# Optimization experiments

Measured on AMD Instinct MI355X. Metric: run time of the kernel, lower is better.

Reference implementation:

```python
import jax, jax.numpy as jnp
import numpy as np

NUM_LAYERS = 3


def setup_inputs() -> dict:
    key = jax.random.key(0)
    k1, k2, k3 = jax.random.split(key, 3)
    B, LT, LC, F = 16, 256, 768, 256
    batch_target = jax.random.normal(k1, (B, LT, F), dtype=jnp.float32)
    batch_claim = jax.random.normal(k2, (B, LC, F), dtype=jnp.float32)
    # adjacency is accepted but mathematically unused (original masked_fill is non-in-place and discarded)
    batch_adj = jax.random.randint(jax.random.fold_in(key, 7), (B, LT + LC, LT + LC), 0, 2, dtype=jnp.int32)
    # per-layer trans_linear weights, nn.Linear(F, F, bias=False): y = x @ W.T, W is [out, in]
    W_trans = jax.random.normal(k3, (NUM_LAYERS, F, F), dtype=jnp.float32) * (1.0 / np.sqrt(F))
    return {"batch_target": batch_target, "batch_claim": batch_claim, "batch_adj": batch_adj, "W_trans": W_trans}


def _gcn_layer(node_rep, W):
    # dot attention: score[b,i,j] = <h_i, h_j>  (symmetric all-pairs dot product)
    # NOTE: original's masked_fill(batch_adj == 0, -1e9) is NOT in-place and its
    # result is discarded, so no masking is applied -- reproduced faithfully here.
    corr = jnp.einsum('bif,bjf->bij', node_rep, node_rep)
    attn = jax.nn.softmax(corr, axis=2)              # softmax over j (dim=2)
    trans = jnp.einsum('blf,gf->blg', node_rep, W)   # trans_linear (bias=False)
    node_out = jax.nn.relu(node_rep + jnp.einsum('bij,bjf->bif', attn, trans))
    return node_out, attn


def reference(batch_target, batch_claim, batch_adj, W_trans):
    target_len = batch_target.shape[1]
    node_rep = jnp.concatenate([batch_target, batch_claim], axis=1)  # [B, L, F]
    all_node_rep, all_corr_score = (), ()
    for i in range(NUM_LAYERS):
        node_rep, corr_score = _gcn_layer(node_rep, W_trans[i])
        all_node_rep = all_node_rep + (node_rep,)
        all_corr_score = all_corr_score + (corr_score,)
        # gcn_dropout: identity in eval mode
    target_rep = node_rep[:, :target_len, :]
    claim_rep = node_rep[:, target_len:, :]
    return (target_rep, claim_rep, all_node_rep, all_corr_score)
```

## Files before the change

### kernel.cpp

```cpp
#include <hip/hip_runtime.h>

typedef _Float16 h16;
typedef _Float16 h16x8 __attribute__((ext_vector_type(8)));
typedef _Float16 h16x4 __attribute__((ext_vector_type(4)));
typedef float    f32x4 __attribute__((ext_vector_type(4)));

#define NBATCH 16
#define LROWS  1024
#define FDIM   256

#define OFF_TGT 0ull
#define OFF_CLM 1048576ull
#define OFF_NR  4194304ull
#define OFF_AT  16777216ull

__device__ __forceinline__ void split2(float x, h16& h, h16& l) {
    h = (h16)x;
    l = (h16)(x - (float)h);
}

typedef const __attribute__((address_space(1))) void gvoid;
typedef __attribute__((address_space(3))) void lvoid;
__device__ __forceinline__ void gl_lds16(const void* g, void* l) {
    __builtin_amdgcn_global_load_lds((gvoid*)g, (lvoid*)l, 16, 0, 0);
}

__device__ const unsigned char TRI_I[36] = {
    0,0,0,0,0,0,0,0, 1,1,1,1,1,1,1, 2,2,2,2,2,2, 3,3,3,3,3, 4,4,4,4, 5,5,5, 6,6, 7};
__device__ const unsigned char TRI_J[36] = {
    0,1,2,3,4,5,6,7, 1,2,3,4,5,6,7, 2,3,4,5,6,7, 3,4,5,6,7, 4,5,6,7, 5,6,7, 6,7, 7};

__global__ __launch_bounds__(256) void convert_all(const float* __restrict__ tgt,
                                                   const float* __restrict__ clm,
                                                   const float* __restrict__ W,
                                                   h16* __restrict__ xh, h16* __restrict__ xl,
                                                   h16* __restrict__ wh) {
    int bid = blockIdx.x;
    if (bid < 4096) {
        size_t e = ((size_t)bid * 256 + threadIdx.x) * 4;
        int b  = (int)(e >> 18);
        int rf = (int)(e & 262143);
        int r  = rf >> 8, f = rf & 255;
        const float* src = (r < 256)
            ? tgt + ((size_t)b << 16) + ((size_t)r << 8) + f
            : clm + (size_t)b * 196608 + ((size_t)(r - 256) << 8) + f;
        f32x4 v = *(const f32x4*)src;
        h16x4 hv, lv;
#pragma unroll
        for (int j = 0; j < 4; ++j) { h16 hh, ll; split2(v[j], hh, ll); hv[j] = hh; lv[j] = ll; }
        *(h16x4*)(xh + e) = hv;
        *(h16x4*)(xl + e) = lv;
    } else {
        size_t e = ((size_t)(bid - 4096) * 256 + threadIdx.x) * 4;
        f32x4 v = *(const f32x4*)(W + e);
        h16x4 hv;
#pragma unroll
        for (int j = 0; j < 4; ++j) hv[j] = (h16)v[j];
        *(h16x4*)(wh + e) = hv;
    }
}

__global__ __launch_bounds__(256, 3) void gemm_ct(
    const h16* __restrict__ Xh, const h16* __restrict__ Xl,
    const h16* __restrict__ Wh,
    h16* __restrict__ Ptil, float2* __restrict__ part,
    h16* __restrict__ Th) {
    const int b = blockIdx.x & 15;
    const int u = blockIdx.x >> 4;
    const bool isCorr = u < 36;
    int it, jt;
    if (isCorr) { it = TRI_I[u]; jt = TRI_J[u]; }
    else        { int v = u - 36; it = v >> 1; jt = v & 1; }
    const int i0 = it * 128;
    const int j0 = jt * 128;
    const int t  = threadIdx.x;
    const int lane = t & 63, wid = t >> 6;
    const int wr = wid >> 1, wc = wid & 1;

    __shared__ alignas(16) char lds[32768];

    const size_t arow = ((size_t)b * LROWS + i0) * 256;
    const h16* bHp; const h16* bLp; size_t brow;
    if (isCorr) { bHp = Xh; bLp = Xl; brow = ((size_t)b * LROWS + j0) * 256; }
    else        { bHp = Wh; bLp = Xl; brow = (size_t)j0 * 256; }

    f32x4 acc[4][4];
#pragma unroll
    for (int i = 0; i < 4; ++i)
#pragma unroll
        for (int j = 0; j < 4; ++j) acc[i][j] = (f32x4){0.f, 0.f, 0.f, 0.f};

    const int grow = t >> 2;
    const int gq   = t & 3;

    for (int kt = 0; kt < 8; ++kt) {
        __syncthreads();
#pragma unroll
        for (int p = 0; p < 2; ++p) {
            int r = p * 64 + grow;
            size_t so = (size_t)r * 256 + kt * 32 + ((gq ^ ((r >> 1) & 3)) << 3);
            char* d = lds + p * 4096 + wid * 1024;
            gl_lds16(Xh + arow + so, d);
            gl_lds16(Xl + arow + so, d + 8192);
            gl_lds16(bHp + brow + so, d + 16384);
            if (isCorr) gl_lds16(bLp + brow + so, d + 24576);
        }
        __syncthreads();

        const int kq = lane >> 4;
        const int rA = wr * 64 + (lane & 15);
        const int rB = wc * 64 + (lane & 15);
        h16x8 ah[4], al[4], bh[4], bl[4];
#pragma unroll
        for (int mi = 0; mi < 4; ++mi) {
            int r   = rA + mi * 16;
            int off = r * 64 + ((kq ^ ((r >> 1) & 3)) << 4);
            ah[mi] = *(const h16x8*)(lds + off);
            al[mi] = *(const h16x8*)(lds + 8192 + off);
        }
#pragma unroll
        for (int nj = 0; nj < 4; ++nj) {
            int r   = rB + nj * 16;
            int off = r * 64 + ((kq ^ ((r >> 1) & 3)) << 4);
            bh[nj] = *(const h16x8*)(lds + 16384 + off);
            if (isCorr) bl[nj] = *(const h16x8*)(lds + 24576 + off);
        }
        __builtin_amdgcn_s_setprio(1);
#pragma unroll
        for (int mi = 0; mi < 4; ++mi)
#pragma unroll
            for (int nj = 0; nj < 4; ++nj) {
                acc[mi][nj] = __builtin_amdgcn_mfma_f32_16x16x32_f16(ah[mi], bh[nj], acc[mi][nj], 0, 0, 0);
                acc[mi][nj] = __builtin_amdgcn_mfma_f32_16x16x32_f16(al[mi], bh[nj], acc[mi][nj], 0, 0, 0);
                if (isCorr)
                    acc[mi][nj] = __builtin_amdgcn_mfma_f32_16x16x32_f16(ah[mi], bl[nj], acc[mi][nj], 0, 0, 0);
            }
        __builtin_amdgcn_s_setprio(0);
    }

    const int mBase = i0 + wr * 64;
    const int nBase = j0 + wc * 64;
    if (isCorr) {
        h16* Pb = Ptil + (size_t)b * LROWS * 1024;
        {
            const int chunk = jt * 2 + wc;
#pragma unroll
            for (int mi = 0; mi < 4; ++mi)
#pragma unroll
                for (int rg = 0; rg < 4; ++rg) {
                    float v0 = acc[mi][0][rg], v1 = acc[mi][1][rg];
                    float v2 = acc[mi][2][rg], v3 = acc[mi][3][rg];
                    float mx = fmaxf(fmaxf(v0, v1), fmaxf(v2, v3));
#pragma unroll
                    for (int off = 8; off >= 1; off >>= 1) mx = fmaxf(mx, __shfl_xor(mx, off, 64));
                    float e0 = __expf(v0 - mx), e1 = __expf(v1 - mx);
                    float e2 = __expf(v2 - mx), e3 = __expf(v3 - mx);
                    float s = e0 + e1 + e2 + e3;
#pragma unroll
                    for (int off = 8; off >= 1; off >>= 1) s += __shfl_xor(s, off, 64);
                    int row = mBase + mi * 16 + ((lane >> 4) * 4) + rg;
                    if ((lane & 15) == 0)
                        part[((size_t)b * 1024 + row) * 16 + chunk] = make_float2(mx, s);
                    size_t rb = (size_t)row * 1024 + nBase + (lane & 15);
                    Pb[rb]      = (h16)e0;
                    Pb[rb + 16] = (h16)e1;
                    Pb[rb + 32] = (h16)e2;
                    Pb[rb + 48] = (h16)e3;
                }
        }
        if (it != jt) {
            const int chunk = it * 2 + wr;
#pragma unroll
            for (int nj = 0; nj < 4; ++nj) {
                float mx = -3.0e38f;
#pragma unroll
                for (int mi = 0; mi < 4; ++mi)
#pragma unroll
                    for (int rg = 0; rg < 4; ++rg) mx = fmaxf(mx, acc[mi][nj][rg]);
                mx = fmaxf(mx, __shfl_xor(mx, 16, 64));
                mx = fmaxf(mx, __shfl_xor(mx, 32, 64));
                float s = 0.f;
                h16x4 pt[4];
#pragma unroll
                for (int mi = 0; mi < 4; ++mi)
#pragma unroll
                    for (int rg = 0; rg < 4; ++rg) {
                        float e = __expf(acc[mi][nj][rg] - mx);
                        s += e;
                        pt[mi][rg] = (h16)e;
                    }
                s += __shfl_xor(s, 16, 64);
                s += __shfl_xor(s, 32, 64);
                int n = nBase + nj * 16 + (lane & 15);
                if (lane < 16)
                    part[((size_t)b * 1024 + n) * 16 + chunk] = make_float2(mx, s);
                size_t nb = (size_t)n * 1024 + mBase + ((lane >> 4) * 4);
#pragma unroll
                for (int mi = 0; mi < 4; ++mi)
                    *(h16x4*)(Pb + nb + mi * 16) = pt[mi];
            }
        }
    } else {
#pragma unroll
        for (int mi = 0; mi < 4; ++mi)
#pragma unroll
            for (int nj = 0; nj < 4; ++nj) {
                int n  = nBase + nj * 16 + (lane & 15);
                int m0 = mBase + mi * 16 + ((lane >> 4) * 4);
                h16x4 hv;
#pragma unroll
                for (int rg = 0; rg < 4; ++rg) hv[rg] = (h16)acc[mi][nj][rg];
                size_t off = ((size_t)b * 256 + n) * 1024 + m0;
                *(h16x4*)(Th + off) = hv;
            }
    }
}

__global__ __launch_bounds__(256, 4) void gemm_pv(
    const h16* __restrict__ Ptil, const float2* __restrict__ part,
    float* __restrict__ At,
    const h16* __restrict__ Th,
    h16* __restrict__ Xh, h16* __restrict__ Xl,
    float* __restrict__ NodeOut, float* __restrict__ OutBase, int last) {
    const int id   = blockIdx.x;
    const int xcd  = id & 7, rest = id >> 3;
    const int b    = (xcd << 1) | (rest & 1);
    const int mt   = rest >> 1;
    const int i0   = mt * 32;
    const int t    = threadIdx.x;
    const int lane = t & 63, wid = t >> 6;
    const int wc   = wid;

    __shared__ alignas(16) char lds[38912];
    float* sc = (float*)(lds + 36864);

    if (t < 32) {
        const float2* pp = part + ((size_t)b * 1024 + i0 + t) * 16;
        float2 v[16];
        float M = -3.0e38f;
#pragma unroll
        for (int c = 0; c < 16; ++c) { v[c] = pp[c]; M = fmaxf(M, v[c].x); }
        float S = 0.f;
#pragma unroll
        for (int c = 0; c < 16; ++c) S += v[c].y * __expf(v[c].x - M);
        float inv = 1.0f / S;
#pragma unroll
        for (int c = 0; c < 16; ++c) sc[t * 16 + c] = __expf(v[c].x - M) * inv;
    }
    __syncthreads();

    const h16* Prow = Ptil + ((size_t)b * LROWS + i0) * 1024;
    float* Arow = At + ((size_t)b * LROWS + i0) * 1024;
    const size_t tbase = (size_t)b * 256 * 1024;

    const int ar = t >> 3;
    const int ac = t & 7;

    f32x4 acc[2][4];
#pragma unroll
    for (int i = 0; i < 2; ++i)
#pragma unroll
        for (int j = 0; j < 4; ++j) acc[i][j] = (f32x4){0.f, 0.f, 0.f, 0.f};

    for (int kt = 0; kt < 16; ++kt) {
        h16x8 pt = *(const h16x8*)(Prow + (size_t)ar * 1024 + kt * 64 + ac * 8);
        float s  = sc[ar * 16 + kt];
        __syncthreads();

#pragma unroll
        for (int itr = 0; itr < 8; ++itr) {
            int g = itr * 32 + ar;
            size_t so = tbase + (size_t)g * 1024 + kt * 64 + ((ac ^ (g & 7)) << 3);
            char* d = lds + 4096 + itr * 4096 + wid * 1024;
            gl_lds16(Th + so, d);
        }

        f32x4 plo, phi;
#pragma unroll
        for (int e = 0; e < 4; ++e) plo[e] = (float)pt[e] * s;
#pragma unroll
        for (int e = 0; e < 4; ++e) phi[e] = (float)pt[4 + e] * s;
        *(f32x4*)(Arow + (size_t)ar * 1024 + kt * 64 + ac * 8)     = plo;
        *(f32x4*)(Arow + (size_t)ar * 1024 + kt * 64 + ac * 8 + 4) = phi;
        h16x8 a16;
#pragma unroll
        for (int e = 0; e < 4; ++e) { a16[e] = (h16)plo[e]; a16[4 + e] = (h16)phi[e]; }
        *(h16x8*)(lds + ar * 128 + ((ac ^ (ar & 7)) << 4)) = a16;
        __syncthreads();

        const int kq = lane >> 4;
        __builtin_amdgcn_s_setprio(1);
#pragma unroll
        for (int s2 = 0; s2 < 2; ++s2) {
            h16x8 ah[2], bh[4];
#pragma unroll
            for (int mi = 0; mi < 2; ++mi) {
                int r = mi * 16 + (lane & 15);
                ah[mi] = *(const h16x8*)(lds + r * 128 + (((s2 * 4 + kq) ^ (r & 7)) << 4));
            }
#pragma unroll
            for (int nf = 0; nf < 4; ++nf) {
                int g = wc * 64 + nf * 16 + (lane & 15);
                bh[nf] = *(const h16x8*)(lds + 4096 + g * 128 + (((s2 * 4 + kq) ^ (g & 7)) << 4));
            }
#pragma unroll
            for (int mi = 0; mi < 2; ++mi)
#pragma unroll
                for (int nf = 0; nf < 4; ++nf)
                    acc[mi][nf] = __builtin_amdgcn_mfma_f32_16x16x32_f16(ah[mi], bh[nf], acc[mi][nf], 0, 0, 0);
        }
        __builtin_amdgcn_s_setprio(0);
    }

#pragma unroll
    for (int mi = 0; mi < 2; ++mi)
#pragma unroll
        for (int nf = 0; nf < 4; ++nf) {
            int n = wc * 64 + nf * 16 + (lane & 15);
#pragma unroll
            for (int rg = 0; rg < 4; ++rg) {
                int m = i0 + mi * 16 + ((lane >> 4) * 4) + rg;
                size_t off = ((size_t)b * LROWS + m) * FDIM + n;
                float res = (float)Xh[off] + (float)Xl[off];
                float y   = res + acc[mi][nf][rg];
                y = y > 0.f ? y : 0.f;
                NodeOut[off] = y;
                h16 hh, ll; split2(y, hh, ll);
                Xh[off] = hh; Xl[off] = ll;
                if (last) {
                    float* dst = (m < 256)
                        ? OutBase + OFF_TGT + ((size_t)b << 16) + ((size_t)m << 8) + n
                        : OutBase + OFF_CLM + (size_t)b * 196608 + ((size_t)(m - 256) << 8) + n;
                    *dst = y;
                }
            }
        }
}

extern "C" void kernel_launch(void* const* d_in, const int* in_sizes, int n_in,
                              void* d_out, int out_size, void* d_ws, size_t ws_size,
                              hipStream_t stream) {
    (void)in_sizes; (void)n_in; (void)out_size; (void)ws_size;
    const float* tgt = (const float*)d_in[0];
    const float* clm = (const float*)d_in[1];
    const float* W   = (const float*)d_in[3];
    float* out = (float*)d_out;
    char*  ws  = (char*)d_ws;

    h16* xh = (h16*)(ws);
    h16* xl = (h16*)(ws + (8ull << 20));
    h16* th = (h16*)(ws + (16ull << 20));
    h16* wh = (h16*)(ws + (24ull << 20));
    float2* part = (float2*)(ws + (25ull << 20));
    h16* ptil = (h16*)(ws + (27ull << 20));

    convert_all<<<4288, 256, 0, stream>>>(tgt, clm, W, xh, xl, wh);

    for (int L = 0; L < 3; ++L) {
        float* at = out + OFF_AT + (size_t)L * 16777216ull;
        float* nr = out + OFF_NR + (size_t)L * 4194304ull;
        gemm_ct<<<832, 256, 0, stream>>>(xh, xl, wh + (size_t)L * 65536, ptil, part, th);
        gemm_pv<<<512, 256, 0, stream>>>(ptil, part, at, th, xh, xl, nr, out, L == 2);
    }
}
```

Before: 227.4 us.

## Stage transposed softmax tile through LDS for coalesced stores and remap batch-to-XCD

The transposed probability tile in the off-diagonal blocks was written to global memory as scattered 8-byte stores. It is now first written into a swizzled LDS buffer, then read back and stored as coalesced 16-byte rows. Separately, the convert and PV kernels change how block IDs map to batch indices, spreading batches across XCDs so each XCD's L2 holds a consistent set of batches. This adds two block-wide barriers and reuses LDS that earlier stages also use, which could add stalls.

```diff
diff --git a/kernel.cpp b/kernel.cpp
--- a/kernel.cpp
+++ b/kernel.cpp
@@ -37,8 +37,10 @@
                                                    h16* __restrict__ wh) {
     int bid = blockIdx.x;
     if (bid < 4096) {
-        size_t e = ((size_t)bid * 256 + threadIdx.x) * 4;
-        int b  = (int)(e >> 18);
+        int b, i;
+        if (bid < 2048) { b = bid & 7;       i = bid >> 3; }
+        else            { b = 8 + (bid & 7); i = (bid - 2048) >> 3; }
+        size_t e = ((size_t)b << 18) + (size_t)i * 1024 + (size_t)threadIdx.x * 4;
         int rf = (int)(e & 262143);
         int r  = rf >> 8, f = rf & 255;
         const float* src = (r < 256)
@@ -169,7 +171,10 @@
                 }
         }
         if (it != jt) {
+            __syncthreads();
             const int chunk = it * 2 + wr;
+            const int cl0 = wc * 64 + (lane & 15);
+            const int r40 = wr * 64 + ((lane >> 4) << 2);
 #pragma unroll
             for (int nj = 0; nj < 4; ++nj) {
                 float mx = -3.0e38f;
@@ -194,10 +199,25 @@
                 int n = nBase + nj * 16 + (lane & 15);
                 if (lane < 16)
                     part[((size_t)b * 1024 + n) * 16 + chunk] = make_float2(mx, s);
-                size_t nb = (size_t)n * 1024 + mBase + ((lane >> 4) * 4);
-#pragma unroll
-                for (int mi = 0; mi < 4; ++mi)
-                    *(h16x4*)(Pb + nb + mi * 16) = pt[mi];
+                const int cl = cl0 + nj * 16;
+#pragma unroll
+                for (int mi = 0; mi < 4; ++mi) {
+                    int r4 = r40 + mi * 16;
+                    *(h16x4*)(lds + cl * 256 + (((r4 ^ ((cl & 7) << 2))) << 1)) = pt[mi];
+                }
+            }
+            __syncthreads();
+#pragma unroll
+            for (int i8 = 0; i8 < 8; ++i8) {
+                int cl = wid * 32 + i8 * 4 + (lane >> 4);
+                int R  = (lane & 15) * 8;
+                int k4 = (cl & 7) << 2;
+                h16x4 v0 = *(const h16x4*)(lds + cl * 256 + (((R    ) ^ k4) << 1));
+                h16x4 v1 = *(const h16x4*)(lds + cl * 256 + (((R + 4) ^ k4) << 1));
+                h16x8 vv;
+                vv[0] = v0[0]; vv[1] = v0[1]; vv[2] = v0[2]; vv[3] = v0[3];
+                vv[4] = v1[0]; vv[5] = v1[1]; vv[6] = v1[2]; vv[7] = v1[3];
+                *(h16x8*)(Pb + (size_t)(j0 + cl) * 1024 + i0 + R) = vv;
             }
         }
     } else {
@@ -223,9 +243,8 @@
     h16* __restrict__ Xh, h16* __restrict__ Xl,
     float* __restrict__ NodeOut, float* __restrict__ OutBase, int last) {
     const int id   = blockIdx.x;
-    const int xcd  = id & 7, rest = id >> 3;
-    const int b    = (xcd << 1) | (rest & 1);
-    const int mt   = rest >> 1;
+    const int b    = (id & 7) | (((id >> 3) & 1) << 3);
+    const int mt   = id >> 4;
     const int i0   = mt * 32;
     const int t    = threadIdx.x;
     const int lane = t & 63, wid = t >> 6;
```

Result: faster. 209.8 us (-7.7%).
